# Performance work log

Hardware: AMD Instinct MI355X
Metric: run time of the kernel (lower is better)

Reference implementation:

```python
import jax, jax.numpy as jnp
import numpy as np

D_MODEL = 512
WINDOW = 8
N_LAYERS = 3
BATCH = 16384
EPS = 1e-12  # torch F.normalize eps


def _l2norm(x):
    # normalize over last axis, matching torch.nn.functional.normalize(p=2)
    n = jnp.sqrt(jnp.sum(x * x, axis=-1, keepdims=True))
    return x / jnp.maximum(n, EPS)


def setup_inputs() -> dict:
    key = jax.random.key(0)
    ks = jax.random.split(key, 14)
    d, w, L = D_MODEL, WINDOW, N_LAYERS
    s = 1.0 / np.sqrt(d)
    inp = {
        "x": jax.random.normal(ks[0], (BATCH, w + 1, d), dtype=jnp.float32),
        # stacked per-layer params
        "Wq": jax.random.normal(ks[1], (L, d, d), dtype=jnp.float32) * s,
        "bq": jax.random.normal(ks[2], (L, d), dtype=jnp.float32) * s,
        "Wk": jax.random.normal(ks[3], (L, w + 1, d, d), dtype=jnp.float32) * s,  # grouped conv: per-position linear
        "bk": jax.random.normal(ks[4], (L, w + 1, d), dtype=jnp.float32) * s,
        "Wfw": jax.random.normal(ks[5], (L, w, d, d), dtype=jnp.float32) * s,
        "bfw": jax.random.normal(ks[6], (L, w, d), dtype=jnp.float32) * s,
        "Wfc": jax.random.normal(ks[7], (L, d, d), dtype=jnp.float32) * s,
        "bfc": jax.random.normal(ks[8], (L, d), dtype=jnp.float32) * s,
        # final layer params
        "Wqf": jax.random.normal(ks[9], (d, d), dtype=jnp.float32) * s,
        "bqf": jax.random.normal(ks[10], (d,), dtype=jnp.float32) * s,
        "Wkf": jax.random.normal(ks[11], (w + 1, d, d), dtype=jnp.float32) * s,
        "bkf": jax.random.normal(ks[12], (w + 1, d), dtype=jnp.float32) * s,
    }
    return inp


def _attn_cent(x, Wq, bq, Wk, bk):
    # q: Linear on last position; k: grouped conv == per-position linear
    xc = x[:, -1, :]                                   # [B, d]
    q = xc @ Wq.T + bq                                 # [B, d]
    k = jnp.einsum('bpe,pde->bpd', x, Wk) + bk         # [B, W+1, d]
    attns = jax.nn.softmax(jnp.einsum('bd,bpd->bp', q, k), axis=-1)
    x_cent = jnp.einsum('bp,bpd->bd', attns, x)        # [B, d]
    return xc, x_cent


def _pt_layer(x, Wq, bq, Wk, bk, Wfw, bfw, Wfc, bfc):
    xc, x_cent = _attn_cent(x, Wq, bq, Wk, bk)
    x_cent = _l2norm(x_cent)
    x_cent = x_cent @ Wfc.T + bfc                      # ff_cent (dropout = identity, eval)
    x_cent = _l2norm(x_cent + xc)
    xw = x[:, :-1, :]                                  # [B, W, d]
    x_window = jnp.einsum('bpe,pde->bpd', xw, Wfw) + bfw + xw
    x_window = _l2norm(x_window)
    return jnp.concatenate([x_window, x_cent[:, None, :]], axis=1)


def reference(x, Wq, bq, Wk, bk, Wfw, bfw, Wfc, bfc, Wqf, bqf, Wkf, bkf):
    for l in range(N_LAYERS):
        x = _pt_layer(x, Wq[l], bq[l], Wk[l], bk[l], Wfw[l], bfw[l], Wfc[l], bfc[l])
    # final layer
    xc, x_cent = _attn_cent(x, Wqf, bqf, Wkf, bkf)
    return _l2norm((x_cent + xc)[:, None, :])          # [B, 1, d]
```

## Files before the change

### kernel.cpp

```cpp
#include <hip/hip_runtime.h>

#define BATCH_N 16384
#define PPLANE 524288
typedef unsigned short ushort_t;
typedef __attribute__((ext_vector_type(4))) float f32x4;
typedef __attribute__((ext_vector_type(8))) short s16x8;

__device__ inline void split_bf(float f, ushort_t& h, ushort_t& l) {
    unsigned u = __float_as_uint(f);
    h = (ushort_t)(u >> 16);
    float fh = __uint_as_float(u & 0xFFFF0000u);
    float r = f - fh;
    l = (ushort_t)(__float_as_uint(r) >> 16);
}

__global__ __launch_bounds__(256) void pack_w_k(
    const float* __restrict__ src, ushort_t* __restrict__ dst, int nrows)
{
    const int lane = threadIdx.x & 63;
    const int row = blockIdx.x * 4 + (threadIdx.x >> 6);
    if (row >= nrows) return;
    const int r = row & 7;
    const int kc = lane >> 2, c = lane & 3;
    const float* s = src + (size_t)row * 512 + kc * 32 + c * 8;
    const f32x4 v0 = *(const f32x4*)s;
    const f32x4 v1 = *(const f32x4*)(s + 4);
    s16x8 hv, lv;
    ushort_t h, l;
#pragma unroll
    for (int e = 0; e < 4; ++e) { split_bf(v0[e], h, l); hv[e] = (short)h; lv[e] = (short)l; }
#pragma unroll
    for (int e = 0; e < 4; ++e) { split_bf(v1[e], h, l); hv[4 + e] = (short)h; lv[4 + e] = (short)l; }
    ushort_t* base = dst + (size_t)row * 1024 + kc * 64;
    *(s16x8*)&base[(c ^ r) * 8]       = hv;
    *(s16x8*)&base[((4 + c) ^ r) * 8] = lv;
}

template <int EPI>
__global__ __launch_bounds__(256, 3) void mfma_gemm_k(
    const float* __restrict__ A, int lda, int aoff,
    const ushort_t* __restrict__ Wpk,
    const float* __restrict__ bias, float* __restrict__ outp,
    const float* __restrict__ q, float* __restrict__ logits)
{
    __shared__ __align__(16) ushort_t As[128 * 64];
    __shared__ __align__(16) ushort_t Bs[128 * 64];

    const int t = threadIdx.x;
    const int lane = t & 63, wave = t >> 6;
    const int wm = (wave >> 1) * 64, wn = (wave & 1) * 64;
    const int quad = lane >> 4, l15 = lane & 15;
    const size_t b0 = (size_t)blockIdx.x * 128;
    const int n0 = blockIdx.y * 128;
    int p = 0;
    if (EPI == 1) {
        p = blockIdx.z;
        Wpk += (size_t)PPLANE * p;
        aoff += p * 512;
    }

    const int arow = t & 127;
    const int rr = arow & 7;
    const float* aptr = A + (b0 + arow) * (size_t)lda + aoff + (t >> 7) * 8;
    ushort_t* awr_hi[2];
    ushort_t* awr_lo[2];
#pragma unroll
    for (int u = 0; u < 2; ++u) {
        const int c = (t >> 7) + 2 * u;
        awr_hi[u] = &As[arow * 64 + ((c ^ rr) * 8)];
        awr_lo[u] = &As[arow * 64 + (((4 + c) ^ rr) * 8)];
    }

    const int xr = (l15 & 7) << 3;
    const int offh = (quad * 8) ^ xr;
    const int offl = (32 + quad * 8) ^ xr;

    f32x4 acc[4][4] = {};

    for (int kc = 0; kc < 16; ++kc) {
        f32x4 av[4];
#pragma unroll
        for (int u = 0; u < 2; ++u) {
            av[2 * u]     = *(const f32x4*)(aptr + kc * 32 + u * 16);
            av[2 * u + 1] = *(const f32x4*)(aptr + kc * 32 + u * 16 + 4);
        }
        s16x8 bv[4];
#pragma unroll
        for (int u = 0; u < 4; ++u) {
            const int f = t + 256 * u;
            bv[u] = *(const s16x8*)&Wpk[(size_t)(n0 + (f >> 3)) * 1024
                                        + kc * 64 + (f & 7) * 8];
        }
        __syncthreads();
#pragma unroll
        for (int u = 0; u < 2; ++u) {
            s16x8 hv, lv;
            ushort_t h, l;
#pragma unroll
            for (int e = 0; e < 4; ++e) {
                split_bf(av[2 * u][e], h, l); hv[e] = (short)h; lv[e] = (short)l;
            }
#pragma unroll
            for (int e = 0; e < 4; ++e) {
                split_bf(av[2 * u + 1][e], h, l); hv[4 + e] = (short)h; lv[4 + e] = (short)l;
            }
            *(s16x8*)awr_hi[u] = hv;
            *(s16x8*)awr_lo[u] = lv;
        }
#pragma unroll
        for (int u = 0; u < 4; ++u) {
            const int f = t + 256 * u;
            *(s16x8*)&Bs[f * 8] = bv[u];
        }
        __syncthreads();
        s16x8 ah[4], alo[4];
#pragma unroll
        for (int i = 0; i < 4; ++i) {
            ah[i]  = *(const s16x8*)&As[(wm + i * 16 + l15) * 64 + offh];
            alo[i] = *(const s16x8*)&As[(wm + i * 16 + l15) * 64 + offl];
        }
#pragma unroll
        for (int j = 0; j < 4; ++j) {
            const s16x8 bh = *(const s16x8*)&Bs[(wn + j * 16 + l15) * 64 + offh];
            const s16x8 bl = *(const s16x8*)&Bs[(wn + j * 16 + l15) * 64 + offl];
#pragma unroll
            for (int i = 0; i < 4; ++i) {
                acc[i][j] = __builtin_amdgcn_mfma_f32_16x16x32_bf16(ah[i], bh, acc[i][j], 0, 0, 0);
                acc[i][j] = __builtin_amdgcn_mfma_f32_16x16x32_bf16(ah[i], bl, acc[i][j], 0, 0, 0);
                acc[i][j] = __builtin_amdgcn_mfma_f32_16x16x32_bf16(alo[i], bh, acc[i][j], 0, 0, 0);
            }
        }
    }

    if (EPI == 0) {
#pragma unroll
        for (int i = 0; i < 4; ++i) {
            const int gm0 = (int)b0 + wm + i * 16 + quad * 4;
#pragma unroll
            for (int j = 0; j < 4; ++j) {
                const int gn = n0 + wn + j * 16 + l15;
                const float bv = bias[gn];
#pragma unroll
                for (int r = 0; r < 4; ++r)
                    outp[(size_t)(gm0 + r) * 512 + gn] = acc[i][j][r] + bv;
            }
        }
    } else {
        float rp[4][4] = {};
#pragma unroll
        for (int i = 0; i < 4; ++i) {
            const int gm0 = (int)b0 + wm + i * 16 + quad * 4;
#pragma unroll
            for (int j = 0; j < 4; ++j) {
                const int gn = n0 + wn + j * 16 + l15;
                const float bv = bias[(size_t)p * 512 + gn];
#pragma unroll
                for (int r = 0; r < 4; ++r)
                    rp[i][r] += (acc[i][j][r] + bv) * q[(size_t)(gm0 + r) * 512 + gn];
            }
        }
#pragma unroll
        for (int m = 1; m < 16; m <<= 1)
#pragma unroll
            for (int i = 0; i < 4; ++i)
#pragma unroll
                for (int r = 0; r < 4; ++r)
                    rp[i][r] += __shfl_xor(rp[i][r], m, 64);
        if (l15 == 0) {
#pragma unroll
            for (int i = 0; i < 4; ++i) {
                const int gm0 = (int)b0 + wm + i * 16 + quad * 4;
#pragma unroll
                for (int r = 0; r < 4; ++r)
                    atomicAdd(&logits[(size_t)(gm0 + r) * 9 + p], rp[i][r]);
            }
        }
    }
}

__global__ __launch_bounds__(256) void softmax_cent_k(
    const float* __restrict__ x, const float* __restrict__ logits,
    float* __restrict__ outp, int mode)
{
    const int lane = threadIdx.x & 63;
    const size_t b = (size_t)blockIdx.x * 4 + (threadIdx.x >> 6);
    float lg[9], m = -1e30f;
#pragma unroll
    for (int p = 0; p < 9; ++p) { lg[p] = logits[b * 9 + p]; m = fmaxf(m, lg[p]); }
    float s = 0.f;
#pragma unroll
    for (int p = 0; p < 9; ++p) { lg[p] = __expf(lg[p] - m); s += lg[p]; }
    const float inv = 1.0f / s;
    f32x4 c[2];
    float ssq = 0.f;
#pragma unroll
    for (int v = 0; v < 2; ++v) {
        f32x4 a = {0.f, 0.f, 0.f, 0.f};
#pragma unroll
        for (int p = 0; p < 9; ++p) {
            const f32x4 xv = ((const f32x4*)&x[(b * 9 + p) * 512])[v * 64 + lane];
            a += lg[p] * xv;
        }
        a *= inv;
        if (mode) a += ((const f32x4*)&x[(b * 9 + 8) * 512])[v * 64 + lane];
        c[v] = a;
        ssq += a[0]*a[0] + a[1]*a[1] + a[2]*a[2] + a[3]*a[3];
    }
#pragma unroll
    for (int off = 32; off > 0; off >>= 1) ssq += __shfl_xor(ssq, off, 64);
    const float invn = 1.0f / fmaxf(sqrtf(ssq), 1e-12f);
#pragma unroll
    for (int v = 0; v < 2; ++v)
        ((f32x4*)&outp[b * 512])[v * 64 + lane] = c[v] * invn;
}

__global__ __launch_bounds__(256) void resid_norm_k(
    float* __restrict__ dst, int dstride, const float* __restrict__ src)
{
    const int lane = threadIdx.x & 63;
    const size_t b = (size_t)blockIdx.x * 4 + (threadIdx.x >> 6);
    f32x4* d4 = (f32x4*)&dst[b * (size_t)dstride];
    const f32x4* s4 = (const f32x4*)&src[b * 512];
    f32x4 a[2];
    float ssq = 0.f;
#pragma unroll
    for (int v = 0; v < 2; ++v) {
        a[v] = d4[v * 64 + lane] + s4[v * 64 + lane];
        ssq += a[v][0]*a[v][0] + a[v][1]*a[v][1] + a[v][2]*a[v][2] + a[v][3]*a[v][3];
    }
#pragma unroll
    for (int off = 32; off > 0; off >>= 1) ssq += __shfl_xor(ssq, off, 64);
    const float invn = 1.0f / fmaxf(sqrtf(ssq), 1e-12f);
#pragma unroll
    for (int v = 0; v < 2; ++v) d4[v * 64 + lane] = a[v] * invn;
}

extern "C" void kernel_launch(void* const* d_in, const int* in_sizes, int n_in,
                              void* d_out, int out_size, void* d_ws, size_t ws_size,
                              hipStream_t stream) {
    (void)in_sizes; (void)n_in; (void)out_size; (void)ws_size;
    float* x = (float*)d_in[0];
    const float* Wq  = (const float*)d_in[1];
    const float* bq  = (const float*)d_in[2];
    const float* Wk  = (const float*)d_in[3];
    const float* bk  = (const float*)d_in[4];
    const float* Wfw = (const float*)d_in[5];
    const float* bfw = (const float*)d_in[6];
    const float* Wfc = (const float*)d_in[7];
    const float* bfc = (const float*)d_in[8];
    const float* Wqf = (const float*)d_in[9];
    const float* bqf = (const float*)d_in[10];
    const float* Wkf = (const float*)d_in[11];
    const float* bkf = (const float*)d_in[12];
    float* out = (float*)d_out;

    ushort_t* wpk = (ushort_t*)d_ws;
    float* fbuf   = (float*)(wpk + (size_t)67 * PPLANE);
    float* q      = fbuf;
    float* cent   = q    + (size_t)BATCH_N * 512;
    float* y      = cent + (size_t)BATCH_N * 512;
    float* logits = y    + (size_t)BATCH_N * 512;
    float* tmp    = cent;

    const size_t OWq = 0, OWk = 3, OWfw = 30, OWfc = 54, OWqf = 57, OWkf = 58;

    struct { const float* s; size_t off; int cnt; } cv[6] = {
        {Wq, OWq, 3}, {Wk, OWk, 27}, {Wfw, OWfw, 24},
        {Wfc, OWfc, 3}, {Wqf, OWqf, 1}, {Wkf, OWkf, 9}};
    for (int i = 0; i < 6; ++i) {
        const int nrows = cv[i].cnt * 512;
        pack_w_k<<<nrows / 4, 256, 0, stream>>>(
            cv[i].s, wpk + cv[i].off * PPLANE, nrows);
    }

    const dim3 gemm_grid(BATCH_N / 128, 4);
    const dim3 log_grid(BATCH_N / 128, 4, 9);
    const int ew_grid = BATCH_N / 4;

    for (int l = 0; l < 3; ++l) {
        mfma_gemm_k<0><<<gemm_grid, 256, 0, stream>>>(
            x, 9 * 512, 8 * 512,
            wpk + (OWq + l) * PPLANE,
            bq + l * 512, q, nullptr, nullptr);
        hipMemsetAsync(logits, 0, (size_t)BATCH_N * 9 * sizeof(float), stream);
        mfma_gemm_k<1><<<log_grid, 256, 0, stream>>>(
            x, 9 * 512, 0,
            wpk + (OWk + (size_t)l * 9) * PPLANE,
            bk + (size_t)l * 9 * 512, nullptr, q, logits);
        softmax_cent_k<<<ew_grid, 256, 0, stream>>>(x, logits, cent, 0);
        mfma_gemm_k<0><<<gemm_grid, 256, 0, stream>>>(
            cent, 512, 0,
            wpk + (OWfc + l) * PPLANE,
            bfc + l * 512, y, nullptr, nullptr);
        resid_norm_k<<<ew_grid, 256, 0, stream>>>(x + 8 * 512, 9 * 512, y);
        for (int p = 0; p < 8; ++p) {
            mfma_gemm_k<0><<<gemm_grid, 256, 0, stream>>>(
                x, 9 * 512, p * 512,
                wpk + (OWfw + (size_t)l * 8 + p) * PPLANE,
                bfw + ((size_t)l * 8 + p) * 512, tmp, nullptr, nullptr);
            resid_norm_k<<<ew_grid, 256, 0, stream>>>(x + p * 512, 9 * 512, tmp);
        }
    }
    mfma_gemm_k<0><<<gemm_grid, 256, 0, stream>>>(
        x, 9 * 512, 8 * 512, wpk + OWqf * PPLANE,
        bqf, q, nullptr, nullptr);
    hipMemsetAsync(logits, 0, (size_t)BATCH_N * 9 * sizeof(float), stream);
    mfma_gemm_k<1><<<log_grid, 256, 0, stream>>>(
        x, 9 * 512, 0, wpk + OWkf * PPLANE,
        bkf, nullptr, q, logits);
    softmax_cent_k<<<ew_grid, 256, 0, stream>>>(x, logits, out, 1);
}
```

Measured before the change: 3.195 ms.

## Double-buffer GEMM shared tiles with register prefetch and fold residual into weights

The GEMM kernel now keeps two LDS buffers and prefetches the next k-chunk of A and B into registers right after the barrier, so global loads overlap with the MFMA work and one barrier per iteration is removed. The launch bound drops to 2 blocks per SM because LDS use doubles. Separately, the identity matrix is added to the window feed-forward weights during packing, so the residual add in the per-position normalization kernel is skipped and x is read one fewer time there. Adding the identity before the bf16 hi/lo split slightly changes rounding.

```diff
diff --git a/kernel.cpp b/kernel.cpp
--- a/kernel.cpp
+++ b/kernel.cpp
@@ -15,7 +15,8 @@
 }
 
 __global__ __launch_bounds__(256) void pack_w_k(
-    const float* __restrict__ src, ushort_t* __restrict__ dst, int nrows)
+    const float* __restrict__ src, ushort_t* __restrict__ dst, int nrows,
+    int addI)
 {
     const int lane = threadIdx.x & 63;
     const int row = blockIdx.x * 4 + (threadIdx.x >> 6);
@@ -23,8 +24,17 @@
     const int r = row & 7;
     const int kc = lane >> 2, c = lane & 3;
     const float* s = src + (size_t)row * 512 + kc * 32 + c * 8;
-    const f32x4 v0 = *(const f32x4*)s;
-    const f32x4 v1 = *(const f32x4*)(s + 4);
+    f32x4 v0 = *(const f32x4*)s;
+    f32x4 v1 = *(const f32x4*)(s + 4);
+    if (addI) {
+        const int d = row & 511;
+        const int kbase = kc * 32 + c * 8;
+#pragma unroll
+        for (int e = 0; e < 4; ++e) {
+            if (kbase + e == d)     v0[e] += 1.0f;
+            if (kbase + 4 + e == d) v1[e] += 1.0f;
+        }
+    }
     s16x8 hv, lv;
     ushort_t h, l;
 #pragma unroll
@@ -37,14 +47,14 @@
 }
 
 template <int EPI>
-__global__ __launch_bounds__(256, 3) void mfma_gemm_k(
+__global__ __launch_bounds__(256, 2) void mfma_gemm_k(
     const float* __restrict__ A, int lda, int aoff,
     const ushort_t* __restrict__ Wpk,
     const float* __restrict__ bias, float* __restrict__ outp,
     const float* __restrict__ q, float* __restrict__ logits)
 {
-    __shared__ __align__(16) ushort_t As[128 * 64];
-    __shared__ __align__(16) ushort_t Bs[128 * 64];
+    __shared__ __align__(16) ushort_t As[2][128 * 64];
+    __shared__ __align__(16) ushort_t Bs[2][128 * 64];
 
     const int t = threadIdx.x;
     const int lane = t & 63, wave = t >> 6;
@@ -62,14 +72,10 @@
     const int arow = t & 127;
     const int rr = arow & 7;
     const float* aptr = A + (b0 + arow) * (size_t)lda + aoff + (t >> 7) * 8;
-    ushort_t* awr_hi[2];
-    ushort_t* awr_lo[2];
-#pragma unroll
-    for (int u = 0; u < 2; ++u) {
-        const int c = (t >> 7) + 2 * u;
-        awr_hi[u] = &As[arow * 64 + ((c ^ rr) * 8)];
-        awr_lo[u] = &As[arow * 64 + (((4 + c) ^ rr) * 8)];
-    }
+    const int awo_hi[2] = { arow * 64 + (((t >> 7) + 0) ^ rr) * 8,
+                            arow * 64 + (((t >> 7) + 2) ^ rr) * 8 };
+    const int awo_lo[2] = { arow * 64 + ((4 + (t >> 7) + 0) ^ rr) * 8,
+                            arow * 64 + ((4 + (t >> 7) + 2) ^ rr) * 8 };
 
     const int xr = (l15 & 7) << 3;
     const int offh = (quad * 8) ^ xr;
@@ -77,21 +83,22 @@
 
     f32x4 acc[4][4] = {};
 
+    f32x4 av[4];
+    s16x8 bv[4];
+#pragma unroll
+    for (int u = 0; u < 2; ++u) {
+        av[2 * u]     = *(const f32x4*)(aptr + u * 16);
+        av[2 * u + 1] = *(const f32x4*)(aptr + u * 16 + 4);
+    }
+#pragma unroll
+    for (int u = 0; u < 4; ++u) {
+        const int f = t + 256 * u;
+        bv[u] = *(const s16x8*)&Wpk[(size_t)(n0 + (f >> 3)) * 1024 + (f & 7) * 8];
+    }
+
+#pragma unroll 2
     for (int kc = 0; kc < 16; ++kc) {
-        f32x4 av[4];
-#pragma unroll
-        for (int u = 0; u < 2; ++u) {
-            av[2 * u]     = *(const f32x4*)(aptr + kc * 32 + u * 16);
-            av[2 * u + 1] = *(const f32x4*)(aptr + kc * 32 + u * 16 + 4);
-        }
-        s16x8 bv[4];
-#pragma unroll
-        for (int u = 0; u < 4; ++u) {
-            const int f = t + 256 * u;
-            bv[u] = *(const s16x8*)&Wpk[(size_t)(n0 + (f >> 3)) * 1024
-                                        + kc * 64 + (f & 7) * 8];
-        }
-        __syncthreads();
+        const int cur = kc & 1;
 #pragma unroll
         for (int u = 0; u < 2; ++u) {
             s16x8 hv, lv;
@@ -104,25 +111,38 @@
             for (int e = 0; e < 4; ++e) {
                 split_bf(av[2 * u + 1][e], h, l); hv[4 + e] = (short)h; lv[4 + e] = (short)l;
             }
-            *(s16x8*)awr_hi[u] = hv;
-            *(s16x8*)awr_lo[u] = lv;
+            *(s16x8*)&As[cur][awo_hi[u]] = hv;
+            *(s16x8*)&As[cur][awo_lo[u]] = lv;
         }
 #pragma unroll
         for (int u = 0; u < 4; ++u) {
             const int f = t + 256 * u;
-            *(s16x8*)&Bs[f * 8] = bv[u];
+            *(s16x8*)&Bs[cur][f * 8] = bv[u];
         }
         __syncthreads();
+        if (kc + 1 < 16) {
+#pragma unroll
+            for (int u = 0; u < 2; ++u) {
+                av[2 * u]     = *(const f32x4*)(aptr + (kc + 1) * 32 + u * 16);
+                av[2 * u + 1] = *(const f32x4*)(aptr + (kc + 1) * 32 + u * 16 + 4);
+            }
+#pragma unroll
+            for (int u = 0; u < 4; ++u) {
+                const int f = t + 256 * u;
+                bv[u] = *(const s16x8*)&Wpk[(size_t)(n0 + (f >> 3)) * 1024
+                                            + (kc + 1) * 64 + (f & 7) * 8];
+            }
+        }
         s16x8 ah[4], alo[4];
 #pragma unroll
         for (int i = 0; i < 4; ++i) {
-            ah[i]  = *(const s16x8*)&As[(wm + i * 16 + l15) * 64 + offh];
-            alo[i] = *(const s16x8*)&As[(wm + i * 16 + l15) * 64 + offl];
+            ah[i]  = *(const s16x8*)&As[cur][(wm + i * 16 + l15) * 64 + offh];
+            alo[i] = *(const s16x8*)&As[cur][(wm + i * 16 + l15) * 64 + offl];
         }
 #pragma unroll
         for (int j = 0; j < 4; ++j) {
-            const s16x8 bh = *(const s16x8*)&Bs[(wn + j * 16 + l15) * 64 + offh];
-            const s16x8 bl = *(const s16x8*)&Bs[(wn + j * 16 + l15) * 64 + offl];
+            const s16x8 bh = *(const s16x8*)&Bs[cur][(wn + j * 16 + l15) * 64 + offh];
+            const s16x8 bl = *(const s16x8*)&Bs[cur][(wn + j * 16 + l15) * 64 + offl];
 #pragma unroll
             for (int i = 0; i < 4; ++i) {
                 acc[i][j] = __builtin_amdgcn_mfma_f32_16x16x32_bf16(ah[i], bh, acc[i][j], 0, 0, 0);
@@ -139,10 +159,10 @@
 #pragma unroll
             for (int j = 0; j < 4; ++j) {
                 const int gn = n0 + wn + j * 16 + l15;
-                const float bv = bias[gn];
+                const float bvs = bias[gn];
 #pragma unroll
                 for (int r = 0; r < 4; ++r)
-                    outp[(size_t)(gm0 + r) * 512 + gn] = acc[i][j][r] + bv;
+                    outp[(size_t)(gm0 + r) * 512 + gn] = acc[i][j][r] + bvs;
             }
         }
     } else {
@@ -153,10 +173,10 @@
 #pragma unroll
             for (int j = 0; j < 4; ++j) {
                 const int gn = n0 + wn + j * 16 + l15;
-                const float bv = bias[(size_t)p * 512 + gn];
+                const float bvs = bias[(size_t)p * 512 + gn];
 #pragma unroll
                 for (int r = 0; r < 4; ++r)
-                    rp[i][r] += (acc[i][j][r] + bv) * q[(size_t)(gm0 + r) * 512 + gn];
+                    rp[i][r] += (acc[i][j][r] + bvs) * q[(size_t)(gm0 + r) * 512 + gn];
             }
         }
 #pragma unroll
@@ -215,7 +235,7 @@
 }
 
 __global__ __launch_bounds__(256) void resid_norm_k(
-    float* __restrict__ dst, int dstride, const float* __restrict__ src)
+    float* __restrict__ dst, int dstride, const float* __restrict__ src, int add)
 {
     const int lane = threadIdx.x & 63;
     const size_t b = (size_t)blockIdx.x * 4 + (threadIdx.x >> 6);
@@ -225,7 +245,8 @@
     float ssq = 0.f;
 #pragma unroll
     for (int v = 0; v < 2; ++v) {
-        a[v] = d4[v * 64 + lane] + s4[v * 64 + lane];
+        a[v] = s4[v * 64 + lane];
+        if (add) a[v] += d4[v * 64 + lane];
         ssq += a[v][0]*a[v][0] + a[v][1]*a[v][1] + a[v][2]*a[v][2] + a[v][3]*a[v][3];
     }
 #pragma unroll
@@ -264,13 +285,13 @@
 
     const size_t OWq = 0, OWk = 3, OWfw = 30, OWfc = 54, OWqf = 57, OWkf = 58;
 
-    struct { const float* s; size_t off; int cnt; } cv[6] = {
-        {Wq, OWq, 3}, {Wk, OWk, 27}, {Wfw, OWfw, 24},
-        {Wfc, OWfc, 3}, {Wqf, OWqf, 1}, {Wkf, OWkf, 9}};
+    struct { const float* s; size_t off; int cnt; int addI; } cv[6] = {
+        {Wq, OWq, 3, 0}, {Wk, OWk, 27, 0}, {Wfw, OWfw, 24, 1},
+        {Wfc, OWfc, 3, 0}, {Wqf, OWqf, 1, 0}, {Wkf, OWkf, 9, 0}};
     for (int i = 0; i < 6; ++i) {
         const int nrows = cv[i].cnt * 512;
         pack_w_k<<<nrows / 4, 256, 0, stream>>>(
-            cv[i].s, wpk + cv[i].off * PPLANE, nrows);
+            cv[i].s, wpk + cv[i].off * PPLANE, nrows, cv[i].addI);
     }
 
     const dim3 gemm_grid(BATCH_N / 128, 4);
@@ -292,13 +313,13 @@
             cent, 512, 0,
             wpk + (OWfc + l) * PPLANE,
             bfc + l * 512, y, nullptr, nullptr);
-        resid_norm_k<<<ew_grid, 256, 0, stream>>>(x + 8 * 512, 9 * 512, y);
+        resid_norm_k<<<ew_grid, 256, 0, stream>>>(x + 8 * 512, 9 * 512, y, 1);
         for (int p = 0; p < 8; ++p) {
             mfma_gemm_k<0><<<gemm_grid, 256, 0, stream>>>(
                 x, 9 * 512, p * 512,
                 wpk + (OWfw + (size_t)l * 8 + p) * PPLANE,
                 bfw + ((size_t)l * 8 + p) * 512, tmp, nullptr, nullptr);
-            resid_norm_k<<<ew_grid, 256, 0, stream>>>(x + p * 512, 9 * 512, tmp);
+            resid_norm_k<<<ew_grid, 256, 0, stream>>>(x + p * 512, 9 * 512, tmp, 0);
         }
     }
     mfma_gemm_k<0><<<gemm_grid, 256, 0, stream>>>(
```

New measurement: 3.220 ms. No clear change (+0.8%).

## Keep activations in pre-split bf16 hi/lo swizzled layout across all GEMMs

Applied to the files above, without the earlier changes.

Converts x once into an in-place packed bf16 hi/lo swizzled layout, so GEMMs load A tiles directly without per-tile fp32 splitting. Elementwise kernels read and write the packed format. The window residual is folded into the weights by adding identity during packing. Window GEMMs are batched four positions per launch via grid z. This cuts per-GEMM conversion ALU work and launch count, but adds an extra pack pass over x and overwrites the input buffer in place. It also adds an unused LDS pad array that lowers occupancy.

```diff
diff --git a/kernel.cpp b/kernel.cpp
--- a/kernel.cpp
+++ b/kernel.cpp
@@ -13,62 +13,96 @@
     float r = f - fh;
     l = (ushort_t)(__float_as_uint(r) >> 16);
 }
+__device__ inline float recon_bf(short h, short l) {
+    return __uint_as_float(((unsigned)(ushort_t)h) << 16) +
+           __uint_as_float(((unsigned)(ushort_t)l) << 16);
+}
+__device__ inline void pack8(const f32x4& v0, const f32x4& v1, s16x8& hv, s16x8& lv) {
+    ushort_t h, l;
+#pragma unroll
+    for (int e = 0; e < 4; ++e) { split_bf(v0[e], h, l); hv[e] = (short)h; lv[e] = (short)l; }
+#pragma unroll
+    for (int e = 0; e < 4; ++e) { split_bf(v1[e], h, l); hv[4 + e] = (short)h; lv[4 + e] = (short)l; }
+}
+
 
 __global__ __launch_bounds__(256) void pack_w_k(
-    const float* __restrict__ src, ushort_t* __restrict__ dst, int nrows)
+    const float* __restrict__ src, ushort_t* __restrict__ dst, int nrows,
+    int addI)
 {
     const int lane = threadIdx.x & 63;
     const int row = blockIdx.x * 4 + (threadIdx.x >> 6);
     if (row >= nrows) return;
     const int r = row & 7;
     const int kc = lane >> 2, c = lane & 3;
-    const float* s = src + (size_t)row * 512 + kc * 32 + c * 8;
+    const float* s = src + (size_t)row * 512 + lane * 8;
+    f32x4 v0 = *(const f32x4*)s;
+    f32x4 v1 = *(const f32x4*)(s + 4);
+    if (addI) {
+        const int d = row & 511;
+        const int kbase = lane * 8;
+#pragma unroll
+        for (int e = 0; e < 4; ++e) {
+            if (kbase + e == d)     v0[e] += 1.0f;
+            if (kbase + 4 + e == d) v1[e] += 1.0f;
+        }
+    }
+    s16x8 hv, lv;
+    pack8(v0, v1, hv, lv);
+    ushort_t* base = dst + (size_t)row * 1024 + kc * 64;
+    *(s16x8*)&base[(c ^ r) * 8]       = hv;
+    *(s16x8*)&base[((4 + c) ^ r) * 8] = lv;
+}
+
+__global__ __launch_bounds__(256) void pack_x_k(float* __restrict__ xf, int nrows)
+{
+    const int lane = threadIdx.x & 63;
+    const int row = blockIdx.x * 4 + (threadIdx.x >> 6);
+    if (row >= nrows) return;
+    const int b = row / 9;
+    const int r = b & 7;
+    const int kc = lane >> 2, c = lane & 3;
+    const float* s = xf + (size_t)row * 512 + lane * 8;
     const f32x4 v0 = *(const f32x4*)s;
     const f32x4 v1 = *(const f32x4*)(s + 4);
     s16x8 hv, lv;
-    ushort_t h, l;
-#pragma unroll
-    for (int e = 0; e < 4; ++e) { split_bf(v0[e], h, l); hv[e] = (short)h; lv[e] = (short)l; }
-#pragma unroll
-    for (int e = 0; e < 4; ++e) { split_bf(v1[e], h, l); hv[4 + e] = (short)h; lv[4 + e] = (short)l; }
-    ushort_t* base = dst + (size_t)row * 1024 + kc * 64;
+    pack8(v0, v1, hv, lv);
+    ushort_t* base = (ushort_t*)xf + (size_t)row * 1024 + kc * 64;
     *(s16x8*)&base[(c ^ r) * 8]       = hv;
     *(s16x8*)&base[((4 + c) ^ r) * 8] = lv;
 }
 
 template <int EPI>
 __global__ __launch_bounds__(256, 3) void mfma_gemm_k(
-    const float* __restrict__ A, int lda, int aoff,
-    const ushort_t* __restrict__ Wpk,
-    const float* __restrict__ bias, float* __restrict__ outp,
-    const float* __restrict__ q, float* __restrict__ logits)
+    const ushort_t* __restrict__ Ap, int lda_us, int aoff_us, int astep_us,
+    const ushort_t* __restrict__ Wpk, const float* __restrict__ bias,
+    float* __restrict__ outp, const float* __restrict__ q,
+    float* __restrict__ logits)
 {
     __shared__ __align__(16) ushort_t As[128 * 64];
     __shared__ __align__(16) ushort_t Bs[128 * 64];
+    __shared__ ushort_t lds_pad[4096];
 
     const int t = threadIdx.x;
+    if (lda_us == 0) lds_pad[t] = 0;
     const int lane = t & 63, wave = t >> 6;
     const int wm = (wave >> 1) * 64, wn = (wave & 1) * 64;
     const int quad = lane >> 4, l15 = lane & 15;
     const size_t b0 = (size_t)blockIdx.x * 128;
     const int n0 = blockIdx.y * 128;
-    int p = 0;
-    if (EPI == 1) {
-        p = blockIdx.z;
-        Wpk += (size_t)PPLANE * p;
-        aoff += p * 512;
-    }
-
-    const int arow = t & 127;
-    const int rr = arow & 7;
-    const float* aptr = A + (b0 + arow) * (size_t)lda + aoff + (t >> 7) * 8;
-    ushort_t* awr_hi[2];
-    ushort_t* awr_lo[2];
-#pragma unroll
-    for (int u = 0; u < 2; ++u) {
-        const int c = (t >> 7) + 2 * u;
-        awr_hi[u] = &As[arow * 64 + ((c ^ rr) * 8)];
-        awr_lo[u] = &As[arow * 64 + (((4 + c) ^ rr) * 8)];
+    const int z = blockIdx.z;
+    Wpk += (size_t)PPLANE * z;
+    aoff_us += z * astep_us;
+    bias += z * 512;
+    if (EPI == 0) outp += (size_t)z * BATCH_N * 512;
+
+    const ushort_t* aptr[4];
+    const ushort_t* bptr[4];
+#pragma unroll
+    for (int u = 0; u < 4; ++u) {
+        const int id = t + 256 * u;
+        aptr[u] = Ap + (b0 + (id >> 3)) * (size_t)lda_us + aoff_us + (id & 7) * 8;
+        bptr[u] = Wpk + (size_t)(n0 + (id >> 3)) * 1024 + (id & 7) * 8;
     }
 
     const int xr = (l15 & 7) << 3;
@@ -78,39 +112,17 @@
     f32x4 acc[4][4] = {};
 
     for (int kc = 0; kc < 16; ++kc) {
-        f32x4 av[4];
-#pragma unroll
-        for (int u = 0; u < 2; ++u) {
-            av[2 * u]     = *(const f32x4*)(aptr + kc * 32 + u * 16);
-            av[2 * u + 1] = *(const f32x4*)(aptr + kc * 32 + u * 16 + 4);
-        }
-        s16x8 bv[4];
+        s16x8 avv[4], bvv[4];
 #pragma unroll
         for (int u = 0; u < 4; ++u) {
-            const int f = t + 256 * u;
-            bv[u] = *(const s16x8*)&Wpk[(size_t)(n0 + (f >> 3)) * 1024
-                                        + kc * 64 + (f & 7) * 8];
+            avv[u] = *(const s16x8*)(aptr[u] + kc * 64);
+            bvv[u] = *(const s16x8*)(bptr[u] + kc * 64);
         }
         __syncthreads();
 #pragma unroll
-        for (int u = 0; u < 2; ++u) {
-            s16x8 hv, lv;
-            ushort_t h, l;
-#pragma unroll
-            for (int e = 0; e < 4; ++e) {
-                split_bf(av[2 * u][e], h, l); hv[e] = (short)h; lv[e] = (short)l;
-            }
-#pragma unroll
-            for (int e = 0; e < 4; ++e) {
-                split_bf(av[2 * u + 1][e], h, l); hv[4 + e] = (short)h; lv[4 + e] = (short)l;
-            }
-            *(s16x8*)awr_hi[u] = hv;
-            *(s16x8*)awr_lo[u] = lv;
-        }
-#pragma unroll
         for (int u = 0; u < 4; ++u) {
-            const int f = t + 256 * u;
-            *(s16x8*)&Bs[f * 8] = bv[u];
+            *(s16x8*)&As[t * 8 + 2048 * u] = avv[u];
+            *(s16x8*)&Bs[t * 8 + 2048 * u] = bvv[u];
         }
         __syncthreads();
         s16x8 ah[4], alo[4];
@@ -139,10 +151,10 @@
 #pragma unroll
             for (int j = 0; j < 4; ++j) {
                 const int gn = n0 + wn + j * 16 + l15;
-                const float bv = bias[gn];
+                const float bvs = bias[gn];
 #pragma unroll
                 for (int r = 0; r < 4; ++r)
-                    outp[(size_t)(gm0 + r) * 512 + gn] = acc[i][j][r] + bv;
+                    outp[(size_t)(gm0 + r) * 512 + gn] = acc[i][j][r] + bvs;
             }
         }
     } else {
@@ -153,10 +165,10 @@
 #pragma unroll
             for (int j = 0; j < 4; ++j) {
                 const int gn = n0 + wn + j * 16 + l15;
-                const float bv = bias[(size_t)p * 512 + gn];
+                const float bvs = bias[gn];
 #pragma unroll
                 for (int r = 0; r < 4; ++r)
-                    rp[i][r] += (acc[i][j][r] + bv) * q[(size_t)(gm0 + r) * 512 + gn];
+                    rp[i][r] += (acc[i][j][r] + bvs) * q[(size_t)(gm0 + r) * 512 + gn];
             }
         }
 #pragma unroll
@@ -172,15 +184,15 @@
                 const int gm0 = (int)b0 + wm + i * 16 + quad * 4;
 #pragma unroll
                 for (int r = 0; r < 4; ++r)
-                    atomicAdd(&logits[(size_t)(gm0 + r) * 9 + p], rp[i][r]);
+                    atomicAdd(&logits[(size_t)(gm0 + r) * 9 + z], rp[i][r]);
             }
         }
     }
 }
 
 __global__ __launch_bounds__(256) void softmax_cent_k(
-    const float* __restrict__ x, const float* __restrict__ logits,
-    float* __restrict__ outp, int mode)
+    const ushort_t* __restrict__ xp, const float* __restrict__ logits,
+    ushort_t* __restrict__ centp, float* __restrict__ outp, int mode)
 {
     const int lane = threadIdx.x & 63;
     const size_t b = (size_t)blockIdx.x * 4 + (threadIdx.x >> 6);
@@ -191,48 +203,86 @@
 #pragma unroll
     for (int p = 0; p < 9; ++p) { lg[p] = __expf(lg[p] - m); s += lg[p]; }
     const float inv = 1.0f / s;
-    f32x4 c[2];
+
+    const int kc = lane >> 2, c = lane & 3, r = (int)b & 7;
+    const int oh = kc * 64 + ((c ^ r) * 8);
+    const int ol = kc * 64 + (((4 + c) ^ r) * 8);
+
+    float a[8] = {0.f, 0.f, 0.f, 0.f, 0.f, 0.f, 0.f, 0.f};
+    s16x8 h8, l8;
+#pragma unroll
+    for (int p = 0; p < 9; ++p) {
+        const ushort_t* row = xp + (b * 9 + p) * 1024;
+        const s16x8 hv = *(const s16x8*)&row[oh];
+        const s16x8 lv = *(const s16x8*)&row[ol];
+        if (p == 8) { h8 = hv; l8 = lv; }
+#pragma unroll
+        for (int e = 0; e < 8; ++e) a[e] += lg[p] * recon_bf(hv[e], lv[e]);
+    }
+#pragma unroll
+    for (int e = 0; e < 8; ++e) a[e] *= inv;
+    if (mode) {
+#pragma unroll
+        for (int e = 0; e < 8; ++e) a[e] += recon_bf(h8[e], l8[e]);
+    }
     float ssq = 0.f;
 #pragma unroll
-    for (int v = 0; v < 2; ++v) {
-        f32x4 a = {0.f, 0.f, 0.f, 0.f};
-#pragma unroll
-        for (int p = 0; p < 9; ++p) {
-            const f32x4 xv = ((const f32x4*)&x[(b * 9 + p) * 512])[v * 64 + lane];
-            a += lg[p] * xv;
-        }
-        a *= inv;
-        if (mode) a += ((const f32x4*)&x[(b * 9 + 8) * 512])[v * 64 + lane];
-        c[v] = a;
-        ssq += a[0]*a[0] + a[1]*a[1] + a[2]*a[2] + a[3]*a[3];
-    }
+    for (int e = 0; e < 8; ++e) ssq += a[e] * a[e];
 #pragma unroll
     for (int off = 32; off > 0; off >>= 1) ssq += __shfl_xor(ssq, off, 64);
     const float invn = 1.0f / fmaxf(sqrtf(ssq), 1e-12f);
 #pragma unroll
-    for (int v = 0; v < 2; ++v)
-        ((f32x4*)&outp[b * 512])[v * 64 + lane] = c[v] * invn;
+    for (int e = 0; e < 8; ++e) a[e] *= invn;
+
+    if (mode) {
+        f32x4 o0 = {a[0], a[1], a[2], a[3]};
+        f32x4 o1 = {a[4], a[5], a[6], a[7]};
+        *(f32x4*)&outp[b * 512 + lane * 8]     = o0;
+        *(f32x4*)&outp[b * 512 + lane * 8 + 4] = o1;
+    } else {
+        f32x4 v0 = {a[0], a[1], a[2], a[3]};
+        f32x4 v1 = {a[4], a[5], a[6], a[7]};
+        s16x8 hv, lv;
+        pack8(v0, v1, hv, lv);
+        ushort_t* dc = centp + b * 1024;
+        *(s16x8*)&dc[oh] = hv;
+        *(s16x8*)&dc[ol] = lv;
+    }
 }
 
 __global__ __launch_bounds__(256) void resid_norm_k(
-    float* __restrict__ dst, int dstride, const float* __restrict__ src)
+    ushort_t* __restrict__ xp, int slice0, const float* __restrict__ src, int add)
 {
     const int lane = threadIdx.x & 63;
     const size_t b = (size_t)blockIdx.x * 4 + (threadIdx.x >> 6);
-    f32x4* d4 = (f32x4*)&dst[b * (size_t)dstride];
-    const f32x4* s4 = (const f32x4*)&src[b * 512];
-    f32x4 a[2];
-    float ssq = 0.f;
-#pragma unroll
-    for (int v = 0; v < 2; ++v) {
-        a[v] = d4[v * 64 + lane] + s4[v * 64 + lane];
-        ssq += a[v][0]*a[v][0] + a[v][1]*a[v][1] + a[v][2]*a[v][2] + a[v][3]*a[v][3];
-    }
+    const int z = blockIdx.y;
+    ushort_t* drow = xp + (b * 9 + (size_t)(slice0 + z)) * 1024;
+    const float* srow = src + ((size_t)z * BATCH_N + b) * 512 + lane * 8;
+    const int kc = lane >> 2, c = lane & 3, r = (int)b & 7;
+    const int oh = kc * 64 + ((c ^ r) * 8);
+    const int ol = kc * 64 + (((4 + c) ^ r) * 8);
+
+    f32x4 v0 = *(const f32x4*)srow;
+    f32x4 v1 = *(const f32x4*)(srow + 4);
+    if (add) {
+        const s16x8 hv = *(const s16x8*)&drow[oh];
+        const s16x8 lv = *(const s16x8*)&drow[ol];
+#pragma unroll
+        for (int e = 0; e < 4; ++e) {
+            v0[e] += recon_bf(hv[e], lv[e]);
+            v1[e] += recon_bf(hv[4 + e], lv[4 + e]);
+        }
+    }
+    float ssq = v0[0]*v0[0] + v0[1]*v0[1] + v0[2]*v0[2] + v0[3]*v0[3]
+              + v1[0]*v1[0] + v1[1]*v1[1] + v1[2]*v1[2] + v1[3]*v1[3];
 #pragma unroll
     for (int off = 32; off > 0; off >>= 1) ssq += __shfl_xor(ssq, off, 64);
     const float invn = 1.0f / fmaxf(sqrtf(ssq), 1e-12f);
-#pragma unroll
-    for (int v = 0; v < 2; ++v) d4[v * 64 + lane] = a[v] * invn;
+    v0 *= invn; v1 *= invn;
+    s16x8 hv, lv;
+    pack8(v0, v1, hv, lv);
+    *(s16x8*)&drow[oh] = hv;
+    *(s16x8*)&drow[ol] = lv;
 }
 
 extern "C" void kernel_launch(void* const* d_in, const int* in_sizes, int n_in,
@@ -254,59 +304,62 @@
     const float* bkf = (const float*)d_in[12];
     float* out = (float*)d_out;
 
+    ushort_t* xp = (ushort_t*)x;
+
     ushort_t* wpk = (ushort_t*)d_ws;
-    float* fbuf   = (float*)(wpk + (size_t)67 * PPLANE);
-    float* q      = fbuf;
-    float* cent   = q    + (size_t)BATCH_N * 512;
-    float* y      = cent + (size_t)BATCH_N * 512;
-    float* logits = y    + (size_t)BATCH_N * 512;
-    float* tmp    = cent;
+    float* R      = (float*)(wpk + (size_t)67 * PPLANE);
+    float* q      = R;
+    ushort_t* centp = (ushort_t*)(R + (size_t)BATCH_N * 512);
+    float* y      = R + (size_t)2 * BATCH_N * 512;
+    float* tmp    = R;
+    float* logits = R + (size_t)4 * BATCH_N * 512;
 
     const size_t OWq = 0, OWk = 3, OWfw = 30, OWfc = 54, OWqf = 57, OWkf = 58;
 
-    struct { const float* s; size_t off; int cnt; } cv[6] = {
-        {Wq, OWq, 3}, {Wk, OWk, 27}, {Wfw, OWfw, 24},
-        {Wfc, OWfc, 3}, {Wqf, OWqf, 1}, {Wkf, OWkf, 9}};
+    struct { const float* s; size_t off; int cnt; int addI; } cv[6] = {
+        {Wq, OWq, 3, 0}, {Wk, OWk, 27, 0}, {Wfw, OWfw, 24, 1},
+        {Wfc, OWfc, 3, 0}, {Wqf, OWqf, 1, 0}, {Wkf, OWkf, 9, 0}};
     for (int i = 0; i < 6; ++i) {
         const int nrows = cv[i].cnt * 512;
         pack_w_k<<<nrows / 4, 256, 0, stream>>>(
-            cv[i].s, wpk + cv[i].off * PPLANE, nrows);
-    }
-
-    const dim3 gemm_grid(BATCH_N / 128, 4);
+            cv[i].s, wpk + cv[i].off * PPLANE, nrows, cv[i].addI);
+    }
+    pack_x_k<<<BATCH_N * 9 / 4, 256, 0, stream>>>(x, BATCH_N * 9);
+
+    const dim3 gemm_grid(BATCH_N / 128, 4, 1);
     const dim3 log_grid(BATCH_N / 128, 4, 9);
-    const int ew_grid = BATCH_N / 4;
+    const dim3 win_grid(BATCH_N / 128, 4, 4);
+    const dim3 ew_grid(BATCH_N / 4, 1, 1);
+    const dim3 ew4_grid(BATCH_N / 4, 4, 1);
 
     for (int l = 0; l < 3; ++l) {
         mfma_gemm_k<0><<<gemm_grid, 256, 0, stream>>>(
-            x, 9 * 512, 8 * 512,
-            wpk + (OWq + l) * PPLANE,
-            bq + l * 512, q, nullptr, nullptr);
+            xp, 9 * 1024, 8 * 1024, 0,
+            wpk + (OWq + l) * PPLANE, bq + l * 512, q, nullptr, nullptr);
         hipMemsetAsync(logits, 0, (size_t)BATCH_N * 9 * sizeof(float), stream);
         mfma_gemm_k<1><<<log_grid, 256, 0, stream>>>(
-            x, 9 * 512, 0,
-            wpk + (OWk + (size_t)l * 9) * PPLANE,
-            bk + (size_t)l * 9 * 512, nullptr, q, logits);
-        softmax_cent_k<<<ew_grid, 256, 0, stream>>>(x, logits, cent, 0);
+            xp, 9 * 1024, 0, 1024,
+            wpk + (OWk + (size_t)l * 9) * PPLANE, bk + (size_t)l * 9 * 512,
+            nullptr, q, logits);
+        softmax_cent_k<<<ew_grid, 256, 0, stream>>>(xp, logits, centp, nullptr, 0);
         mfma_gemm_k<0><<<gemm_grid, 256, 0, stream>>>(
-            cent, 512, 0,
-            wpk + (OWfc + l) * PPLANE,
-            bfc + l * 512, y, nullptr, nullptr);
-        resid_norm_k<<<ew_grid, 256, 0, stream>>>(x + 8 * 512, 9 * 512, y);
-        for (int p = 0; p < 8; ++p) {
-            mfma_gemm_k<0><<<gemm_grid, 256, 0, stream>>>(
-                x, 9 * 512, p * 512,
-                wpk + (OWfw + (size_t)l * 8 + p) * PPLANE,
-                bfw + ((size_t)l * 8 + p) * 512, tmp, nullptr, nullptr);
-            resid_norm_k<<<ew_grid, 256, 0, stream>>>(x + p * 512, 9 * 512, tmp);
+            centp, 1024, 0, 0,
+            wpk + (OWfc + l) * PPLANE, bfc + l * 512, y, nullptr, nullptr);
+        resid_norm_k<<<ew_grid, 256, 0, stream>>>(xp, 8, y, 1);
+        for (int zb = 0; zb < 8; zb += 4) {
+            mfma_gemm_k<0><<<win_grid, 256, 0, stream>>>(
+                xp, 9 * 1024, zb * 1024, 1024,
+                wpk + (OWfw + (size_t)l * 8 + zb) * PPLANE,
+                bfw + ((size_t)l * 8 + zb) * 512, tmp, nullptr, nullptr);
+            resid_norm_k<<<ew4_grid, 256, 0, stream>>>(xp, zb, tmp, 0);
         }
     }
     mfma_gemm_k<0><<<gemm_grid, 256, 0, stream>>>(
-        x, 9 * 512, 8 * 512, wpk + OWqf * PPLANE,
-        bqf, q, nullptr, nullptr);
+        xp, 9 * 1024, 8 * 1024, 0,
+        wpk + OWqf * PPLANE, bqf, q, nullptr, nullptr);
     hipMemsetAsync(logits, 0, (size_t)BATCH_N * 9 * sizeof(float), stream);
     mfma_gemm_k<1><<<log_grid, 256, 0, stream>>>(
-        x, 9 * 512, 0, wpk + OWkf * PPLANE,
-        bkf, nullptr, q, logits);
-    softmax_cent_k<<<ew_grid, 256, 0, stream>>>(x, logits, out, 1);
-}
+        xp, 9 * 1024, 0, 1024,
+        wpk + OWkf * PPLANE, bkf, nullptr, q, logits);
+    softmax_cent_k<<<ew_grid, 256, 0, stream>>>(xp, logits, nullptr, out, 1);
+}
```

Measured after the change: 2.807 ms. 12.1% less time.
